# Kernel optimization log

Measured on AMD Instinct MI355X. Metric: run time of the kernel, lower is better.

Reference implementation:

```python
import jax, jax.numpy as jnp
import numpy as np

N = 100_000   # nodes
E = 1_600_000 # edges (avg degree 16)
D = 128       # in_dim == emb_dim
L = 3         # num_layer
G = 64        # num graphs in batch
EPS = 1e-5    # batchnorm eps


def setup_inputs() -> dict:
    key = jax.random.key(0)
    ks = jax.random.split(key, 8)
    x = jax.random.normal(ks[0], (N, D), dtype=jnp.float32)
    edge_index = jax.random.randint(ks[1], (2, E), 0, N)
    edge_weight = jax.random.uniform(ks[2], (E,), dtype=jnp.float32)
    batch = jnp.sort(jax.random.randint(ks[3], (N,), 0, G))
    # GCNConv linear weights (in->out) per layer, bias, and BatchNorm affine params
    W = jax.random.normal(ks[4], (L, D, D), dtype=jnp.float32) * 0.05
    b = jnp.zeros((L, D), jnp.float32)
    gamma = jnp.ones((L, D), jnp.float32)
    beta = jnp.zeros((L, D), jnp.float32)
    return dict(x=x, edge_index=edge_index, edge_weight=edge_weight,
                batch=batch, W=W, b=b, gamma=gamma, beta=beta)


def reference(x, edge_index, edge_weight, batch, W, b, gamma, beta):
    # --- GCN normalization with self loops (PyG gcn_norm, fill_value=1) ---
    loop = jnp.arange(N)
    src = jnp.concatenate([edge_index[0], loop])
    dst = jnp.concatenate([edge_index[1], loop])
    ew = jnp.concatenate([edge_weight, jnp.ones((N,), x.dtype)])
    deg = jax.ops.segment_sum(ew, dst, num_segments=N)            # [N]
    dinv = jnp.where(deg > 0, jax.lax.rsqrt(jnp.maximum(deg, 1e-12)), 0.0)
    norm = dinv[src] * ew * dinv[dst]                              # [E+N]

    for i in range(L):
        h = x @ W[i]                                               # [N, D] linear (no bias in lin)
        msg = h[src] * norm[:, None]                               # gather + scale
        out = jax.ops.segment_sum(msg, dst, num_segments=N) + b[i] # scatter-add + conv bias
        # BatchNorm1d (training-mode batch stats, biased var)
        mu = out.mean(axis=0)
        var = jnp.mean((out - mu) ** 2, axis=0)
        out = gamma[i] * (out - mu) * jax.lax.rsqrt(var + EPS) + beta[i]
        x = jax.nn.relu(out)                                       # dropout p=0 -> identity

    # sum pooling over graphs (last layer only; concat=False)
    return jax.ops.segment_sum(x, batch, num_segments=G)           # [G, D]
```

## Files before the change

kernel.cpp:

```cpp
#include <hip/hip_runtime.h>

#define NN 100000
#define NE 1600000
#define DD 128
#define NL 3
#define NG 64
#define EPSBN 1e-5f
#define NBUCK 196
#define NAGG (NN / 16)

typedef __attribute__((ext_vector_type(8))) short short8v;
typedef __attribute__((ext_vector_type(4))) float float4v;
typedef __attribute__((ext_vector_type(2))) float float2v;

__device__ inline void atomAddF(float* p, float v) {
#if defined(__AMDGCN__)
    unsafeAtomicAdd(p, v);
#else
    atomicAdd(p, v);
#endif
}

__device__ inline ushort f2bf(float f) {
    uint u = __float_as_uint(f);
    uint r = ((u >> 16) & 1u) + 0x7fffu;
    return (ushort)((u + r) >> 16);
}

__device__ inline uint f2fp8(float f) {
    return (uint)__builtin_amdgcn_cvt_pk_fp8_f32(f, f, 0, false) & 0xffu;
}

__device__ inline void accf8(float (&acc)[8], uint2 g, float wgt) {
    float2v p0 = __builtin_amdgcn_cvt_pk_f32_fp8(g.x, false);
    float2v p1 = __builtin_amdgcn_cvt_pk_f32_fp8(g.x, true);
    float2v p2 = __builtin_amdgcn_cvt_pk_f32_fp8(g.y, false);
    float2v p3 = __builtin_amdgcn_cvt_pk_f32_fp8(g.y, true);
    acc[0] = fmaf(wgt, p0[0], acc[0]);
    acc[1] = fmaf(wgt, p0[1], acc[1]);
    acc[2] = fmaf(wgt, p1[0], acc[2]);
    acc[3] = fmaf(wgt, p1[1], acc[3]);
    acc[4] = fmaf(wgt, p2[0], acc[4]);
    acc[5] = fmaf(wgt, p2[1], acc[5]);
    acc[6] = fmaf(wgt, p3[0], acc[6]);
    acc[7] = fmaf(wgt, p3[1], acc[7]);
}

__global__ __launch_bounds__(256) void k_zero_fo(const float* __restrict__ W,
                                                 ushort* __restrict__ Wt,
                                                 float* __restrict__ out,
                                                 float* __restrict__ stats,
                                                 int* __restrict__ gbcnt) {
    int i = blockIdx.x * 256 + threadIdx.x;
    if (i < NL * DD * DD) {
        int l = i >> 14, r = i & 16383;
        int k = r >> 7, n = r & 127;
        Wt[(size_t)l * DD * DD + n * DD + k] = f2bf(W[i]);
        return;
    }
    int j = i - NL * DD * DD;
    if (j < NG * DD) { out[j] = 0.f; return; }
    j -= NG * DD;
    if (j < 768) { stats[j] = 0.f; return; }
    j -= 768;
    if (j < NBUCK) gbcnt[j] = 0;
}

__global__ __launch_bounds__(256) void k_bcnt(const int* __restrict__ ei,
                                              int* __restrict__ gbcnt) {
    __shared__ int lh[NBUCK];
    int tid = threadIdx.x;
    if (tid < NBUCK) lh[tid] = 0;
    __syncthreads();
    for (int e = blockIdx.x * 256 + tid; e < NE; e += 256 * 256)
        atomicAdd(&lh[ei[NE + e] >> 9], 1);
    __syncthreads();
    if (tid < NBUCK) atomicAdd(&gbcnt[tid], lh[tid]);
}

__global__ __launch_bounds__(256) void k_bscan(const int* __restrict__ gbcnt,
                                               int* __restrict__ boff,
                                               int* __restrict__ gcur) {
    __shared__ int s[256];
    int t = threadIdx.x;
    int v = (t < NBUCK) ? gbcnt[t] : 0;
    s[t] = v;
    __syncthreads();
    for (int off = 1; off < 256; off <<= 1) {
        int add = (t >= off) ? s[t - off] : 0;
        __syncthreads();
        s[t] += add;
        __syncthreads();
    }
    if (t < NBUCK) {
        int ex = s[t] - v;
        boff[t] = ex;
        gcur[t] = ex;
    }
    if (t == NBUCK - 1) boff[NBUCK] = s[t];
}

__global__ __launch_bounds__(256) void k_bscatter(const int* __restrict__ ei,
                                                  const float* __restrict__ ew,
                                                  int* __restrict__ gcur,
                                                  int2* __restrict__ srcw) {
    __shared__ int hist[NBUCK], base[NBUCK], cur[NBUCK];
    const int tid = threadIdx.x;
    const int e0 = blockIdx.x * 6250, e1 = e0 + 6250;
    if (tid < NBUCK) hist[tid] = 0;
    __syncthreads();
    for (int e = e0 + tid; e < e1; e += 256)
        atomicAdd(&hist[ei[NE + e] >> 9], 1);
    __syncthreads();
    if (tid < NBUCK) {
        base[tid] = atomicAdd(&gcur[tid], hist[tid]);
        cur[tid] = 0;
    }
    __syncthreads();
    for (int e = e0 + tid; e < e1; e += 256) {
        int d = ei[NE + e];
        int b = d >> 9;
        int p = base[b] + atomicAdd(&cur[b], 1);
        int2 sw;
        sw.x = ei[e] | ((d & 511) << 17);
        sw.y = __float_as_int(ew[e]);
        srcw[p] = sw;
    }
}

__global__ __launch_bounds__(256) void k_bsort(const int2* __restrict__ srcw,
                                               const int* __restrict__ boff,
                                               int* __restrict__ row_off,
                                               int2* __restrict__ csr,
                                               float* __restrict__ dinv) {
    __shared__ int h0[512], h1[512], exc[512], cur[512];
    __shared__ float degacc[512];
    const int tid = threadIdx.x;
    const int b = blockIdx.x;
    const int p0 = boff[b], p1 = boff[b + 1];
    const int nbn = min(512, NN - (b << 9));

    for (int i = tid; i < 512; i += 256) {
        h0[i] = 0;
        degacc[i] = 0.f;
    }
    __syncthreads();
    for (int p = p0 + tid; p < p1; p += 256)
        atomicAdd(&h0[(srcw[p].x >> 17) & 511], 1);
    __syncthreads();

    int* sA = h0;
    int* sB = h1;
    for (int off = 1; off < 512; off <<= 1) {
        for (int i = tid; i < 512; i += 256) {
            int v = sA[i];
            if (i >= off) v += sA[i - off];
            sB[i] = v;
        }
        __syncthreads();
        int* tp = sA; sA = sB; sB = tp;
    }
    for (int i = tid; i < 512; i += 256) {
        exc[i] = (i == 0) ? 0 : sA[i - 1];
        cur[i] = 0;
    }
    __syncthreads();

    for (int n = tid; n < nbn; n += 256)
        row_off[(b << 9) + n] = p0 + exc[n];
    if (b == NBUCK - 1 && tid == 0) row_off[NN] = NE;

    for (int p = p0 + tid; p < p1; p += 256) {
        int2 sw = srcw[p];
        int dl = (sw.x >> 17) & 511;
        int q = p0 + exc[dl] + atomicAdd(&cur[dl], 1);
        int2 outv;
        outv.x = sw.x & 0x1FFFF;
        outv.y = sw.y;
        csr[q] = outv;
        atomicAdd(&degacc[dl], __int_as_float(sw.y));
    }
    __syncthreads();
    for (int n = tid; n < nbn; n += 256)
        dinv[(b << 9) + n] = rsqrtf(1.0f + degacc[n]);
}

__global__ __launch_bounds__(256) void k_nrm2(int2* __restrict__ csr,
                                              const int* __restrict__ row_off,
                                              const float* __restrict__ dinv) {
    int node = blockIdx.x * 256 + threadIdx.x;
    if (node >= NN) return;
    int beg = row_off[node], end = row_off[node + 1];
    float dv = dinv[node];
    int* y = (int*)csr;
    for (int j = beg; j < end; ++j) {
        int2 e = csr[j];
        float nw = dv * __int_as_float(e.y) * dinv[e.x];
        y[2 * (size_t)j + 1] = __float_as_int(nw);
    }
}

__global__ __launch_bounds__(256, 3) void k_gemm4(const float* __restrict__ X,
                                                  const ushort* __restrict__ Xb,
                                                  const ushort* __restrict__ Wt,
                                                  const float* __restrict__ stats,
                                                  const float* __restrict__ gamma,
                                                  const float* __restrict__ beta,
                                                  int applyBN,
                                                  unsigned char* __restrict__ H) {
    __shared__ ushort ws[128 * 128];
    __shared__ ushort xs[64 * 128];
    __shared__ float scs[DD], shs[DD];
    const int tid = threadIdx.x;

    for (int c = tid; c < 2048; c += 256) {
        int n = c >> 4, k8 = (c & 15) * 8;
        uint4 w = *(const uint4*)&Wt[n * DD + k8];
        int idx = n * 128 + (((k8 * 2) ^ ((n & 7) << 4)) >> 1);
        *(uint4*)&ws[idx] = w;
    }
    if (applyBN && tid < DD) {
        float mu = stats[tid] * (1.0f / NN);
        float var = stats[DD + tid] * (1.0f / NN) - mu * mu;
        float inv = rsqrtf(var + EPSBN);
        float s = gamma[tid] * inv;
        scs[tid] = s;
        shs[tid] = beta[tid] - mu * s;
    }

    const int wid = tid >> 6, lane = tid & 63;
    const int wm = wid >> 1, wn = wid & 1;
    const int lrow = lane & 15, lk = lane >> 4;

#pragma unroll
    for (int t = 0; t < 2; ++t) {
        int row0 = (blockIdx.x * 2 + t) * 64;
        if (row0 >= NN) break;
        __syncthreads();

        for (int c = tid; c < 1024; c += 256) {
            int r = c >> 4, k8 = (c & 15) * 8;
            int gr = row0 + r;
            float v[8];
            if (applyBN) {
                uint4 g = (gr < NN) ? *(const uint4*)&Xb[(size_t)gr * DD + k8]
                                    : make_uint4(0u, 0u, 0u, 0u);
                v[0] = __uint_as_float(g.x << 16);
                v[1] = __uint_as_float(g.x & 0xffff0000u);
                v[2] = __uint_as_float(g.y << 16);
                v[3] = __uint_as_float(g.y & 0xffff0000u);
                v[4] = __uint_as_float(g.z << 16);
                v[5] = __uint_as_float(g.z & 0xffff0000u);
                v[6] = __uint_as_float(g.w << 16);
                v[7] = __uint_as_float(g.w & 0xffff0000u);
#pragma unroll
                for (int i = 0; i < 8; ++i)
                    v[i] = fmaxf(fmaf(v[i], scs[k8 + i], shs[k8 + i]), 0.f);
            } else {
                if (gr < NN) {
                    float4 a = *(const float4*)&X[(size_t)gr * DD + k8];
                    float4 b = *(const float4*)&X[(size_t)gr * DD + k8 + 4];
                    v[0] = a.x; v[1] = a.y; v[2] = a.z; v[3] = a.w;
                    v[4] = b.x; v[5] = b.y; v[6] = b.z; v[7] = b.w;
                } else {
#pragma unroll
                    for (int i = 0; i < 8; ++i) v[i] = 0.f;
                }
            }
            uint4 st;
            st.x = (uint)f2bf(v[0]) | ((uint)f2bf(v[1]) << 16);
            st.y = (uint)f2bf(v[2]) | ((uint)f2bf(v[3]) << 16);
            st.z = (uint)f2bf(v[4]) | ((uint)f2bf(v[5]) << 16);
            st.w = (uint)f2bf(v[6]) | ((uint)f2bf(v[7]) << 16);
            int idx = r * 128 + (((k8 * 2) ^ ((r & 7) << 4)) >> 1);
            *(uint4*)&xs[idx] = st;
        }
        __syncthreads();

        float4v acc[2][4];
#pragma unroll
        for (int i = 0; i < 2; ++i)
#pragma unroll
            for (int j = 0; j < 4; ++j) acc[i][j] = (float4v){0.f, 0.f, 0.f, 0.f};

#pragma unroll
        for (int ks = 0; ks < 4; ++ks) {
            int kbyte = ks * 64 + lk * 16;
            short8v a[2], b[4];
#pragma unroll
            for (int mg = 0; mg < 2; ++mg) {
                int r = wm * 32 + mg * 16 + lrow;
                a[mg] = *(const short8v*)&xs[r * 128 + ((kbyte ^ ((r & 7) << 4)) >> 1)];
            }
#pragma unroll
            for (int ng = 0; ng < 4; ++ng) {
                int n = wn * 64 + ng * 16 + lrow;
                b[ng] = *(const short8v*)&ws[n * 128 + ((kbyte ^ ((n & 7) << 4)) >> 1)];
            }
#pragma unroll
            for (int mg = 0; mg < 2; ++mg)
#pragma unroll
                for (int ng = 0; ng < 4; ++ng)
                    acc[mg][ng] = __builtin_amdgcn_mfma_f32_16x16x32_bf16(
                        a[mg], b[ng], acc[mg][ng], 0, 0, 0);
        }

#pragma unroll
        for (int mg = 0; mg < 2; ++mg) {
            int rbase = row0 + wm * 32 + mg * 16 + lk * 4;
#pragma unroll
            for (int j = 0; j < 4; ++j) {
                int gr = rbase + j;
                if (gr < NN) {
#pragma unroll
                    for (int ng = 0; ng < 4; ++ng) {
                        int col = wn * 64 + ng * 16 + lrow;
                        H[(size_t)gr * DD + col] = (unsigned char)f2fp8(acc[mg][ng][j]);
                    }
                }
            }
        }
    }
}

__global__ __launch_bounds__(256) void k_agg3(const int2* __restrict__ csr,
                                              const int* __restrict__ row_off,
                                              const float* __restrict__ dinv,
                                              const unsigned char* __restrict__ H,
                                              ushort* __restrict__ Ab,
                                              float* __restrict__ partial) {
    __shared__ float sbv[16][128];
    __shared__ float sbq[16][128];
    const int tid = threadIdx.x;
    int node = blockIdx.x * 16 + (tid >> 4);
    int h = tid & 15;
    int beg = row_off[node], end = row_off[node + 1];
    float dv = dinv[node];
    size_t cb = (size_t)node * DD + h * 8;
    float acc[8] = {0.f, 0.f, 0.f, 0.f, 0.f, 0.f, 0.f, 0.f};
    {
        uint2 v = *(const uint2*)&H[cb];
        accf8(acc, v, dv * dv);
    }

    int j = beg;
    for (; j + 8 <= end; j += 8) {
        int2 e0 = csr[j], e1 = csr[j + 1], e2 = csr[j + 2], e3 = csr[j + 3];
        int2 e4 = csr[j + 4], e5 = csr[j + 5], e6 = csr[j + 6], e7 = csr[j + 7];
        uint2 g0 = *(const uint2*)&H[(size_t)e0.x * DD + h * 8];
        uint2 g1 = *(const uint2*)&H[(size_t)e1.x * DD + h * 8];
        uint2 g2 = *(const uint2*)&H[(size_t)e2.x * DD + h * 8];
        uint2 g3 = *(const uint2*)&H[(size_t)e3.x * DD + h * 8];
        uint2 g4 = *(const uint2*)&H[(size_t)e4.x * DD + h * 8];
        uint2 g5 = *(const uint2*)&H[(size_t)e5.x * DD + h * 8];
        uint2 g6 = *(const uint2*)&H[(size_t)e6.x * DD + h * 8];
        uint2 g7 = *(const uint2*)&H[(size_t)e7.x * DD + h * 8];
        accf8(acc, g0, __int_as_float(e0.y));
        accf8(acc, g1, __int_as_float(e1.y));
        accf8(acc, g2, __int_as_float(e2.y));
        accf8(acc, g3, __int_as_float(e3.y));
        accf8(acc, g4, __int_as_float(e4.y));
        accf8(acc, g5, __int_as_float(e5.y));
        accf8(acc, g6, __int_as_float(e6.y));
        accf8(acc, g7, __int_as_float(e7.y));
    }
    for (; j + 4 <= end; j += 4) {
        int2 e0 = csr[j], e1 = csr[j + 1], e2 = csr[j + 2], e3 = csr[j + 3];
        uint2 g0 = *(const uint2*)&H[(size_t)e0.x * DD + h * 8];
        uint2 g1 = *(const uint2*)&H[(size_t)e1.x * DD + h * 8];
        uint2 g2 = *(const uint2*)&H[(size_t)e2.x * DD + h * 8];
        uint2 g3 = *(const uint2*)&H[(size_t)e3.x * DD + h * 8];
        accf8(acc, g0, __int_as_float(e0.y));
        accf8(acc, g1, __int_as_float(e1.y));
        accf8(acc, g2, __int_as_float(e2.y));
        accf8(acc, g3, __int_as_float(e3.y));
    }
    for (; j < end; ++j) {
        int2 e = csr[j];
        uint2 g = *(const uint2*)&H[(size_t)e.x * DD + h * 8];
        accf8(acc, g, __int_as_float(e.y));
    }

    uint4 st;
    st.x = (uint)f2bf(acc[0]) | ((uint)f2bf(acc[1]) << 16);
    st.y = (uint)f2bf(acc[2]) | ((uint)f2bf(acc[3]) << 16);
    st.z = (uint)f2bf(acc[4]) | ((uint)f2bf(acc[5]) << 16);
    st.w = (uint)f2bf(acc[6]) | ((uint)f2bf(acc[7]) << 16);
    *(uint4*)&Ab[cb] = st;

    int n = tid >> 4, c0 = h * 8;
#pragma unroll
    for (int i = 0; i < 8; ++i) {
        float a = acc[i];
        sbv[n][c0 + i] = a;
        sbq[n][c0 + i] = a * a;
    }
    __syncthreads();
    float s = 0.f;
    if (tid < 128) {
#pragma unroll
        for (int k = 0; k < 16; ++k) s += sbv[k][tid];
    } else {
        int c = tid - 128;
#pragma unroll
        for (int k = 0; k < 16; ++k) s += sbq[k][c];
    }
    partial[(size_t)blockIdx.x * 256 + tid] = s;
}

__global__ __launch_bounds__(256) void k_bn_red(const float* __restrict__ partial,
                                                float* __restrict__ stats) {
    int r0 = blockIdx.x * 25;
    int r1 = min(r0 + 25, NAGG);
    int t = threadIdx.x;
    float s = 0.f;
    for (int r = r0; r < r1; ++r) s += partial[(size_t)r * 256 + t];
    atomAddF(&stats[t], s);
}

__global__ __launch_bounds__(256) void k_pool(const ushort* __restrict__ Ab,
                                              const int* __restrict__ batch,
                                              const float* __restrict__ stats,
                                              const float* __restrict__ gamma,
                                              const float* __restrict__ beta,
                                              float* __restrict__ out) {
    __shared__ int bsh[512];
    __shared__ float scs[DD], shs[DD];
    const int tid = threadIdx.x;
    const int lane = tid & 15, rg = tid >> 4;
    const int c0 = lane * 8;
    const int v0 = blockIdx.x * 512;
    const int v1 = min(v0 + 512, NN);
    for (int i = tid; i < v1 - v0; i += 256) bsh[i] = batch[v0 + i];
    if (tid < DD) {
        float mu = stats[tid] * (1.0f / NN);
        float var = stats[DD + tid] * (1.0f / NN) - mu * mu;
        float inv = rsqrtf(var + EPSBN);
        float s = gamma[tid] * inv;
        scs[tid] = s;
        shs[tid] = beta[tid] - mu * s;
    }
    __syncthreads();

    float s[8], t[8];
#pragma unroll
    for (int i = 0; i < 8; ++i) {
        s[i] = scs[c0 + i];
        t[i] = shs[c0 + i];
    }
    float acc[8] = {0.f, 0.f, 0.f, 0.f, 0.f, 0.f, 0.f, 0.f};
    int g = -1;
    for (int v = v0 + rg; v < v1; v += 16) {
        int bg = bsh[v - v0];
        if (bg != g) {
            if (g >= 0) {
                float* op = &out[(size_t)g * DD + c0];
#pragma unroll
                for (int i = 0; i < 8; ++i) atomAddF(op + i, acc[i]);
            }
            g = bg;
#pragma unroll
            for (int i = 0; i < 8; ++i) acc[i] = 0.f;
        }
        uint4 a = *(const uint4*)&Ab[(size_t)v * DD + c0];
        float x0 = __uint_as_float(a.x << 16);
        float x1 = __uint_as_float(a.x & 0xffff0000u);
        float x2 = __uint_as_float(a.y << 16);
        float x3 = __uint_as_float(a.y & 0xffff0000u);
        float x4 = __uint_as_float(a.z << 16);
        float x5 = __uint_as_float(a.z & 0xffff0000u);
        float x6 = __uint_as_float(a.w << 16);
        float x7 = __uint_as_float(a.w & 0xffff0000u);
        acc[0] += fmaxf(fmaf(x0, s[0], t[0]), 0.f);
        acc[1] += fmaxf(fmaf(x1, s[1], t[1]), 0.f);
        acc[2] += fmaxf(fmaf(x2, s[2], t[2]), 0.f);
        acc[3] += fmaxf(fmaf(x3, s[3], t[3]), 0.f);
        acc[4] += fmaxf(fmaf(x4, s[4], t[4]), 0.f);
        acc[5] += fmaxf(fmaf(x5, s[5], t[5]), 0.f);
        acc[6] += fmaxf(fmaf(x6, s[6], t[6]), 0.f);
        acc[7] += fmaxf(fmaf(x7, s[7], t[7]), 0.f);
    }
    if (g >= 0) {
        float* op = &out[(size_t)g * DD + c0];
#pragma unroll
        for (int i = 0; i < 8; ++i) atomAddF(op + i, acc[i]);
    }
}

extern "C" void kernel_launch(void* const* d_in, const int* in_sizes, int n_in,
                              void* d_out, int out_size, void* d_ws, size_t ws_size,
                              hipStream_t stream) {
    const float* x     = (const float*)d_in[0];
    const int*   ei    = (const int*)d_in[1];
    const float* ew    = (const float*)d_in[2];
    const int*   batch = (const int*)d_in[3];
    const float* W     = (const float*)d_in[4];
    const float* gamma = (const float*)d_in[6];
    const float* beta  = (const float*)d_in[7];
    float* out = (float*)d_out;

    float* wsp   = (float*)d_ws;
    float* dinv  = wsp;
    float* stats = dinv + NN;
    ushort* Wt   = (ushort*)(stats + 768);
    unsigned char* H = (unsigned char*)(Wt + (size_t)NL * DD * DD);
    ushort* Ab   = (ushort*)(H + (size_t)NN * DD);
    int2*  srcw  = (int2*)(Ab + (size_t)NN * DD);
    float* partial = (float*)(srcw + NE);
    int*   row_off = (int*)(partial + (size_t)NAGG * 256);
    int*   gbcnt = row_off + NN + 4;
    int*   boff  = gbcnt + NBUCK;
    int*   gcur  = boff + NBUCK + 4;
    int2*  csr   = (int2*)(gcur + NBUCK);

    k_zero_fo<<<(NL * DD * DD + NG * DD + 768 + NBUCK + 255) / 256, 256, 0,
                stream>>>(W, Wt, out, stats, gbcnt);

    k_bcnt<<<256, 256, 0, stream>>>(ei, gbcnt);
    k_bscan<<<1, 256, 0, stream>>>(gbcnt, boff, gcur);
    k_bscatter<<<256, 256, 0, stream>>>(ei, ew, gcur, srcw);
    k_bsort<<<NBUCK, 256, 0, stream>>>(srcw, boff, row_off, csr, dinv);
    k_nrm2<<<(NN + 255) / 256, 256, 0, stream>>>(csr, row_off, dinv);

    for (int l = 0; l < NL; ++l) {
        const float* st_prev = stats + (l - 1) * 256;
        const float* ga_prev = gamma + (size_t)(l > 0 ? l - 1 : 0) * DD;
        const float* be_prev = beta + (size_t)(l > 0 ? l - 1 : 0) * DD;
        k_gemm4<<<(NN + 127) / 128, 256, 0, stream>>>(
            x, Ab, Wt + (size_t)l * DD * DD, l > 0 ? st_prev : stats,
            ga_prev, be_prev, l > 0 ? 1 : 0, H);
        k_agg3<<<NAGG, 256, 0, stream>>>(csr, row_off, dinv, H, Ab, partial);
        k_bn_red<<<(NAGG + 24) / 25, 256, 0, stream>>>(partial, stats + l * 256);
    }

    k_pool<<<NBUCK, 256, 0, stream>>>(Ab, batch, stats + 2 * 256,
                                      gamma + 2 * DD, beta + 2 * DD, out);
}
```

Measured before the change: 343.0 us.

## Fold edge normalization into aggregation and load GEMM A operand directly to registers

Removes the separate k_nrm2 pass that rewrote per-edge normalized weights. The aggregation kernel now multiplies each raw edge weight by dinv[src] on the fly and scales the whole accumulator by dinv[dst] once at the end. The GEMM is also restructured: each wave loads its 16-row A fragment straight from global memory into registers, skipping the LDS staging buffer and its barriers. It uses 64-row blocks with 8 column tiles per wave and a launch bound of 4 blocks. The trade-off is an extra dinv gather per edge in every layer's aggregation, and less coalesced A loads in the GEMM.

```diff
diff --git a/kernel.cpp b/kernel.cpp
--- a/kernel.cpp
+++ b/kernel.cpp
@@ -185,22 +185,7 @@
         dinv[(b << 9) + n] = rsqrtf(1.0f + degacc[n]);
 }
 
-__global__ __launch_bounds__(256) void k_nrm2(int2* __restrict__ csr,
-                                              const int* __restrict__ row_off,
-                                              const float* __restrict__ dinv) {
-    int node = blockIdx.x * 256 + threadIdx.x;
-    if (node >= NN) return;
-    int beg = row_off[node], end = row_off[node + 1];
-    float dv = dinv[node];
-    int* y = (int*)csr;
-    for (int j = beg; j < end; ++j) {
-        int2 e = csr[j];
-        float nw = dv * __int_as_float(e.y) * dinv[e.x];
-        y[2 * (size_t)j + 1] = __float_as_int(nw);
-    }
-}
-
-__global__ __launch_bounds__(256, 3) void k_gemm4(const float* __restrict__ X,
+__global__ __launch_bounds__(256, 4) void k_gemm5(const float* __restrict__ X,
                                                   const ushort* __restrict__ Xb,
                                                   const ushort* __restrict__ Wt,
                                                   const float* __restrict__ stats,
@@ -209,7 +194,6 @@
                                                   int applyBN,
                                                   unsigned char* __restrict__ H) {
     __shared__ ushort ws[128 * 128];
-    __shared__ ushort xs[64 * 128];
     __shared__ float scs[DD], shs[DD];
     const int tid = threadIdx.x;
 
@@ -227,98 +211,70 @@
         scs[tid] = s;
         shs[tid] = beta[tid] - mu * s;
     }
+    __syncthreads();
 
     const int wid = tid >> 6, lane = tid & 63;
-    const int wm = wid >> 1, wn = wid & 1;
     const int lrow = lane & 15, lk = lane >> 4;
-
-#pragma unroll
-    for (int t = 0; t < 2; ++t) {
-        int row0 = (blockIdx.x * 2 + t) * 64;
-        if (row0 >= NN) break;
-        __syncthreads();
-
-        for (int c = tid; c < 1024; c += 256) {
-            int r = c >> 4, k8 = (c & 15) * 8;
-            int gr = row0 + r;
-            float v[8];
-            if (applyBN) {
-                uint4 g = (gr < NN) ? *(const uint4*)&Xb[(size_t)gr * DD + k8]
-                                    : make_uint4(0u, 0u, 0u, 0u);
-                v[0] = __uint_as_float(g.x << 16);
-                v[1] = __uint_as_float(g.x & 0xffff0000u);
-                v[2] = __uint_as_float(g.y << 16);
-                v[3] = __uint_as_float(g.y & 0xffff0000u);
-                v[4] = __uint_as_float(g.z << 16);
-                v[5] = __uint_as_float(g.z & 0xffff0000u);
-                v[6] = __uint_as_float(g.w << 16);
-                v[7] = __uint_as_float(g.w & 0xffff0000u);
-#pragma unroll
-                for (int i = 0; i < 8; ++i)
-                    v[i] = fmaxf(fmaf(v[i], scs[k8 + i], shs[k8 + i]), 0.f);
+    const int gr_a = blockIdx.x * 64 + wid * 16 + lrow;
+
+    float4v acc[8];
+#pragma unroll
+    for (int i = 0; i < 8; ++i) acc[i] = (float4v){0.f, 0.f, 0.f, 0.f};
+
+#pragma unroll
+    for (int ks = 0; ks < 4; ++ks) {
+        const int k8 = ks * 32 + lk * 8;
+        float v[8];
+        if (applyBN) {
+            uint4 g = (gr_a < NN) ? *(const uint4*)&Xb[(size_t)gr_a * DD + k8]
+                                  : make_uint4(0u, 0u, 0u, 0u);
+            v[0] = __uint_as_float(g.x << 16);
+            v[1] = __uint_as_float(g.x & 0xffff0000u);
+            v[2] = __uint_as_float(g.y << 16);
+            v[3] = __uint_as_float(g.y & 0xffff0000u);
+            v[4] = __uint_as_float(g.z << 16);
+            v[5] = __uint_as_float(g.z & 0xffff0000u);
+            v[6] = __uint_as_float(g.w << 16);
+            v[7] = __uint_as_float(g.w & 0xffff0000u);
+#pragma unroll
+            for (int i = 0; i < 8; ++i)
+                v[i] = fmaxf(fmaf(v[i], scs[k8 + i], shs[k8 + i]), 0.f);
+        } else {
+            if (gr_a < NN) {
+                float4 a0 = *(const float4*)&X[(size_t)gr_a * DD + k8];
+                float4 a1 = *(const float4*)&X[(size_t)gr_a * DD + k8 + 4];
+                v[0] = a0.x; v[1] = a0.y; v[2] = a0.z; v[3] = a0.w;
+                v[4] = a1.x; v[5] = a1.y; v[6] = a1.z; v[7] = a1.w;
             } else {
-                if (gr < NN) {
-                    float4 a = *(const float4*)&X[(size_t)gr * DD + k8];
-                    float4 b = *(const float4*)&X[(size_t)gr * DD + k8 + 4];
-                    v[0] = a.x; v[1] = a.y; v[2] = a.z; v[3] = a.w;
-                    v[4] = b.x; v[5] = b.y; v[6] = b.z; v[7] = b.w;
-                } else {
-#pragma unroll
-                    for (int i = 0; i < 8; ++i) v[i] = 0.f;
-                }
+#pragma unroll
+                for (int i = 0; i < 8; ++i) v[i] = 0.f;
             }
-            uint4 st;
-            st.x = (uint)f2bf(v[0]) | ((uint)f2bf(v[1]) << 16);
-            st.y = (uint)f2bf(v[2]) | ((uint)f2bf(v[3]) << 16);
-            st.z = (uint)f2bf(v[4]) | ((uint)f2bf(v[5]) << 16);
-            st.w = (uint)f2bf(v[6]) | ((uint)f2bf(v[7]) << 16);
-            int idx = r * 128 + (((k8 * 2) ^ ((r & 7) << 4)) >> 1);
-            *(uint4*)&xs[idx] = st;
         }
-        __syncthreads();
-
-        float4v acc[2][4];
-#pragma unroll
-        for (int i = 0; i < 2; ++i)
-#pragma unroll
-            for (int j = 0; j < 4; ++j) acc[i][j] = (float4v){0.f, 0.f, 0.f, 0.f};
-
-#pragma unroll
-        for (int ks = 0; ks < 4; ++ks) {
-            int kbyte = ks * 64 + lk * 16;
-            short8v a[2], b[4];
-#pragma unroll
-            for (int mg = 0; mg < 2; ++mg) {
-                int r = wm * 32 + mg * 16 + lrow;
-                a[mg] = *(const short8v*)&xs[r * 128 + ((kbyte ^ ((r & 7) << 4)) >> 1)];
-            }
-#pragma unroll
-            for (int ng = 0; ng < 4; ++ng) {
-                int n = wn * 64 + ng * 16 + lrow;
-                b[ng] = *(const short8v*)&ws[n * 128 + ((kbyte ^ ((n & 7) << 4)) >> 1)];
-            }
-#pragma unroll
-            for (int mg = 0; mg < 2; ++mg)
-#pragma unroll
-                for (int ng = 0; ng < 4; ++ng)
-                    acc[mg][ng] = __builtin_amdgcn_mfma_f32_16x16x32_bf16(
-                        a[mg], b[ng], acc[mg][ng], 0, 0, 0);
+        uint4 ap;
+        ap.x = (uint)f2bf(v[0]) | ((uint)f2bf(v[1]) << 16);
+        ap.y = (uint)f2bf(v[2]) | ((uint)f2bf(v[3]) << 16);
+        ap.z = (uint)f2bf(v[4]) | ((uint)f2bf(v[5]) << 16);
+        ap.w = (uint)f2bf(v[6]) | ((uint)f2bf(v[7]) << 16);
+        short8v a = *(short8v*)&ap;
+
+        const int kbyte = ks * 64 + lk * 16;
+#pragma unroll
+        for (int ng = 0; ng < 8; ++ng) {
+            int n = ng * 16 + lrow;
+            short8v b = *(const short8v*)&ws[n * 128 + ((kbyte ^ ((n & 7) << 4)) >> 1)];
+            acc[ng] = __builtin_amdgcn_mfma_f32_16x16x32_bf16(a, b, acc[ng], 0, 0, 0);
         }
-
-#pragma unroll
-        for (int mg = 0; mg < 2; ++mg) {
-            int rbase = row0 + wm * 32 + mg * 16 + lk * 4;
-#pragma unroll
-            for (int j = 0; j < 4; ++j) {
-                int gr = rbase + j;
-                if (gr < NN) {
-#pragma unroll
-                    for (int ng = 0; ng < 4; ++ng) {
-                        int col = wn * 64 + ng * 16 + lrow;
-                        H[(size_t)gr * DD + col] = (unsigned char)f2fp8(acc[mg][ng][j]);
-                    }
-                }
-            }
+    }
+
+    const int rbase = blockIdx.x * 64 + wid * 16 + lk * 4;
+#pragma unroll
+    for (int ng = 0; ng < 8; ++ng) {
+        int col = ng * 16 + lrow;
+#pragma unroll
+        for (int j = 0; j < 4; ++j) {
+            int gr = rbase + j;
+            if (gr < NN)
+                H[(size_t)gr * DD + col] = (unsigned char)f2fp8(acc[ng][j]);
         }
     }
 }
@@ -340,13 +296,21 @@
     float acc[8] = {0.f, 0.f, 0.f, 0.f, 0.f, 0.f, 0.f, 0.f};
     {
         uint2 v = *(const uint2*)&H[cb];
-        accf8(acc, v, dv * dv);
+        accf8(acc, v, dv);
     }
 
     int j = beg;
     for (; j + 8 <= end; j += 8) {
         int2 e0 = csr[j], e1 = csr[j + 1], e2 = csr[j + 2], e3 = csr[j + 3];
         int2 e4 = csr[j + 4], e5 = csr[j + 5], e6 = csr[j + 6], e7 = csr[j + 7];
+        float w0 = __int_as_float(e0.y) * dinv[e0.x];
+        float w1 = __int_as_float(e1.y) * dinv[e1.x];
+        float w2 = __int_as_float(e2.y) * dinv[e2.x];
+        float w3 = __int_as_float(e3.y) * dinv[e3.x];
+        float w4 = __int_as_float(e4.y) * dinv[e4.x];
+        float w5 = __int_as_float(e5.y) * dinv[e5.x];
+        float w6 = __int_as_float(e6.y) * dinv[e6.x];
+        float w7 = __int_as_float(e7.y) * dinv[e7.x];
         uint2 g0 = *(const uint2*)&H[(size_t)e0.x * DD + h * 8];
         uint2 g1 = *(const uint2*)&H[(size_t)e1.x * DD + h * 8];
         uint2 g2 = *(const uint2*)&H[(size_t)e2.x * DD + h * 8];
@@ -355,31 +319,39 @@
         uint2 g5 = *(const uint2*)&H[(size_t)e5.x * DD + h * 8];
         uint2 g6 = *(const uint2*)&H[(size_t)e6.x * DD + h * 8];
         uint2 g7 = *(const uint2*)&H[(size_t)e7.x * DD + h * 8];
-        accf8(acc, g0, __int_as_float(e0.y));
-        accf8(acc, g1, __int_as_float(e1.y));
-        accf8(acc, g2, __int_as_float(e2.y));
-        accf8(acc, g3, __int_as_float(e3.y));
-        accf8(acc, g4, __int_as_float(e4.y));
-        accf8(acc, g5, __int_as_float(e5.y));
-        accf8(acc, g6, __int_as_float(e6.y));
-        accf8(acc, g7, __int_as_float(e7.y));
+        accf8(acc, g0, w0);
+        accf8(acc, g1, w1);
+        accf8(acc, g2, w2);
+        accf8(acc, g3, w3);
+        accf8(acc, g4, w4);
+        accf8(acc, g5, w5);
+        accf8(acc, g6, w6);
+        accf8(acc, g7, w7);
     }
     for (; j + 4 <= end; j += 4) {
         int2 e0 = csr[j], e1 = csr[j + 1], e2 = csr[j + 2], e3 = csr[j + 3];
+        float w0 = __int_as_float(e0.y) * dinv[e0.x];
+        float w1 = __int_as_float(e1.y) * dinv[e1.x];
+        float w2 = __int_as_float(e2.y) * dinv[e2.x];
+        float w3 = __int_as_float(e3.y) * dinv[e3.x];
         uint2 g0 = *(const uint2*)&H[(size_t)e0.x * DD + h * 8];
         uint2 g1 = *(const uint2*)&H[(size_t)e1.x * DD + h * 8];
         uint2 g2 = *(const uint2*)&H[(size_t)e2.x * DD + h * 8];
         uint2 g3 = *(const uint2*)&H[(size_t)e3.x * DD + h * 8];
-        accf8(acc, g0, __int_as_float(e0.y));
-        accf8(acc, g1, __int_as_float(e1.y));
-        accf8(acc, g2, __int_as_float(e2.y));
-        accf8(acc, g3, __int_as_float(e3.y));
+        accf8(acc, g0, w0);
+        accf8(acc, g1, w1);
+        accf8(acc, g2, w2);
+        accf8(acc, g3, w3);
     }
     for (; j < end; ++j) {
         int2 e = csr[j];
+        float w = __int_as_float(e.y) * dinv[e.x];
         uint2 g = *(const uint2*)&H[(size_t)e.x * DD + h * 8];
-        accf8(acc, g, __int_as_float(e.y));
-    }
+        accf8(acc, g, w);
+    }
+
+#pragma unroll
+    for (int i = 0; i < 8; ++i) acc[i] *= dv;
 
     uint4 st;
     st.x = (uint)f2bf(acc[0]) | ((uint)f2bf(acc[1]) << 16);
@@ -520,13 +492,12 @@
     k_bscan<<<1, 256, 0, stream>>>(gbcnt, boff, gcur);
     k_bscatter<<<256, 256, 0, stream>>>(ei, ew, gcur, srcw);
     k_bsort<<<NBUCK, 256, 0, stream>>>(srcw, boff, row_off, csr, dinv);
-    k_nrm2<<<(NN + 255) / 256, 256, 0, stream>>>(csr, row_off, dinv);
 
     for (int l = 0; l < NL; ++l) {
         const float* st_prev = stats + (l - 1) * 256;
         const float* ga_prev = gamma + (size_t)(l > 0 ? l - 1 : 0) * DD;
         const float* be_prev = beta + (size_t)(l > 0 ? l - 1 : 0) * DD;
-        k_gemm4<<<(NN + 127) / 128, 256, 0, stream>>>(
+        k_gemm5<<<(NN + 63) / 64, 256, 0, stream>>>(
             x, Ab, Wt + (size_t)l * DD * DD, l > 0 ? st_prev : stats,
             ga_prev, be_prev, l > 0 ? 1 : 0, H);
         k_agg3<<<NAGG, 256, 0, stream>>>(csr, row_off, dinv, H, Ab, partial);
```

Result: faster. 316.0 us (-7.9%).
